# Kernel optimization log

Measured on AMD Instinct MI355X. Metric: run time of the kernel, lower is better.

## Reference

```python
import jax, jax.numpy as jnp
import numpy as np

DN = ('NHWC', 'HWIO', 'NHWC')
EPS = 1e-3  # Keras BatchNormalization default epsilon


def conv2d(x, w):
    return jax.lax.conv_general_dilated(x, w, (1, 1), 'SAME', dimension_numbers=DN)


def hard_sigmoid(x):
    # Keras ConvLSTM2D default recurrent_activation
    return jnp.clip(0.2 * x + 0.5, 0.0, 1.0)


def convlstm2d(x, Wx, Wh, b):
    """Keras ConvLSTM2D, return_sequences=True. x: (B,T,H,W,C).
    Wx: (3,3,C,4F) input kernel, Wh: (3,3,F,4F) recurrent kernel, b: (4F,).
    Gate order (Keras): i, f, c, o."""
    B, T, H, W, C = x.shape
    F = Wh.shape[2]
    # input-to-gate convs for all timesteps in one batched conv
    xg = conv2d(x.reshape(B * T, H, W, C), Wx) + b          # (B*T,H,W,4F)
    xg = xg.reshape(B, T, H, W, 4 * F).transpose(1, 0, 2, 3, 4)  # (T,B,H,W,4F)

    def step(carry, xg_t):
        h, c = carry
        g = xg_t + conv2d(h, Wh)                            # (B,H,W,4F)
        i, f, cc, o = jnp.split(g, 4, axis=-1)
        i = hard_sigmoid(i)
        f = hard_sigmoid(f)
        o = hard_sigmoid(o)
        c = f * c + i * jnp.tanh(cc)
        h = o * jnp.tanh(c)
        return (h, c), h

    h0 = jnp.zeros((B, H, W, F), x.dtype)
    (_, _), hs = jax.lax.scan(step, (h0, h0), xg)           # hs: (T,B,H,W,F)
    return hs.transpose(1, 0, 2, 3, 4)


def batchnorm(x, gamma, beta):
    # training-mode BN over all axes except channel (last)
    mu = x.mean(axis=(0, 1, 2, 3), keepdims=True)
    var = x.var(axis=(0, 1, 2, 3), keepdims=True)
    return gamma * (x - mu) * jax.lax.rsqrt(var + EPS) + beta


def setup_inputs() -> dict:
    key = jax.random.key(0)
    B, T, H, W, C = 4, 8, 16, 16, 256
    F = 256
    ks = jax.random.split(key, 10)
    s = 0.02
    inp = {
        'input_tensor': jax.random.normal(ks[0], (B, T, H, W, C), jnp.float32),
        'Wx1': jax.random.normal(ks[1], (3, 3, C, 4 * F), jnp.float32) * s,
        'Wh1': jax.random.normal(ks[2], (3, 3, F, 4 * F), jnp.float32) * s,
        'b1': jnp.zeros((4 * F,), jnp.float32),
        'g1': jnp.ones((F,), jnp.float32),
        'be1': jnp.zeros((F,), jnp.float32),
        'Wx2': jax.random.normal(ks[3], (3, 3, F, 4 * F), jnp.float32) * s,
        'Wh2': jax.random.normal(ks[4], (3, 3, F, 4 * F), jnp.float32) * s,
        'b2': jnp.zeros((4 * F,), jnp.float32),
        'g2': jnp.ones((F,), jnp.float32),
        'be2': jnp.zeros((F,), jnp.float32),
        'Wx3': jax.random.normal(ks[5], (3, 3, F, 4 * F), jnp.float32) * s,
        'Wh3': jax.random.normal(ks[6], (3, 3, F, 4 * F), jnp.float32) * s,
        'b3': jnp.zeros((4 * F,), jnp.float32),
        'g3': jnp.ones((F,), jnp.float32),
        'be3': jnp.zeros((F,), jnp.float32),
    }
    return inp


def reference(input_tensor, Wx1, Wh1, b1, g1, be1,
              Wx2, Wh2, b2, g2, be2,
              Wx3, Wh3, b3, g3, be3):
    x = batchnorm(convlstm2d(input_tensor, Wx1, Wh1, b1), g1, be1)
    x = batchnorm(convlstm2d(x, Wx2, Wh2, b2), g2, be2)
    x = batchnorm(convlstm2d(x, Wx3, Wh3, b3), g3, be3)
    return x
```

## Files before the change

### kernel.cpp

```cpp
#include <hip/hip_runtime.h>

#define HW      256
#define COUT    1024
#define TSTEPS  8
#define BN_EPS  1e-3f
#define KTOT    2304

typedef unsigned short u16;
typedef unsigned int   u32;
typedef __attribute__((ext_vector_type(8))) _Float16 v8h;
typedef __attribute__((ext_vector_type(4))) float v4f;

__device__ __forceinline__ u16 f2h(float x) {
    _Float16 h = (_Float16)x; return *(u16*)&h;
}
__device__ __forceinline__ float h2f(u16 u) {
    _Float16 h = *(_Float16*)&u; return (float)h;
}
__device__ __forceinline__ float hsig(float x) {
    return fminf(fmaxf(0.2f * x + 0.5f, 0.f), 1.f);
}

typedef __attribute__((address_space(1))) const unsigned int gas_u32;
typedef __attribute__((address_space(3))) unsigned int las_u32;
__device__ __forceinline__ void gl16(const void* g, void* l) {
    __builtin_amdgcn_global_load_lds((gas_u32*)g, (las_u32*)l, 16, 0, 0);
}

__global__ __launch_bounds__(256, 2) void conv_big_k(
    const u16* __restrict__ apad,
    const u16* __restrict__ wT,
    const float* __restrict__ bias,
    u16* __restrict__ out)
{
    constexpr int KQ = 36;
    __shared__ u16 lds[2 * 16384];

    const int bid = blockIdx.x;
    const int xcd = bid & 7, idx = bid >> 3;
    const int by = (xcd >> 1) * 2 + (idx & 1);
    const int bx = (xcd & 1) * 32 + (idx >> 1);
    const int m0 = bx * 128, n0 = by * 128;
    const int tid = threadIdx.x, lane = tid & 63, w = tid >> 6;
    const int wr = w >> 1, wc = w & 1;
    const int lr = lane >> 3;
    const int g  = (lane & 7) ^ lr;
    const int fr = lane & 15, kc = lane >> 4;

    const char* a_src[4];
    #pragma unroll
    for (int i = 0; i < 4; ++i) {
        int m = m0 + w * 32 + i * 8 + lr;
        int img = m >> 8, pix = m & 255, yy = pix >> 4, xx = pix & 15;
        a_src[i] = (const char*)apad + ((((long)img * 18 + yy) * 18 + xx) * 256 + g * 8) * 2;
    }
    const char* b_src[4];
    #pragma unroll
    for (int i = 0; i < 4; ++i) {
        int n = n0 + w * 32 + i * 8 + lr;
        b_src[i] = (const char*)wT + ((long)n * KTOT + g * 8) * 2;
    }

    int aro[4][2], bro[4][2];
    #pragma unroll
    for (int mi = 0; mi < 4; ++mi) {
        int rl = wr * 64 + mi * 16 + fr;
        #pragma unroll
        for (int ks = 0; ks < 2; ++ks)
            aro[mi][ks] = rl * 128 + ((((ks << 2) | kc) ^ (fr & 7)) << 4);
    }
    #pragma unroll
    for (int ni = 0; ni < 4; ++ni) {
        int nr = wc * 64 + ni * 16 + fr;
        #pragma unroll
        for (int ks = 0; ks < 2; ++ks)
            bro[ni][ks] = 16384 + nr * 128 + ((((ks << 2) | kc) ^ (fr & 7)) << 4);
    }

    v4f acc[4][4];
    #pragma unroll
    for (int mi = 0; mi < 4; ++mi)
        #pragma unroll
        for (int ni = 0; ni < 4; ++ni) acc[mi][ni] = (v4f)0.f;

#define STAGE_B(J) { int j_ = (J); int dxy = j_ >> 2, c64 = j_ & 3;           \
    int dy = (dxy * 11) >> 5; int dx = dxy - dy * 3;                          \
    int aoff = ((dy * 18 + dx) * 256 + c64 * 64) * 2; int boff = j_ * 128;    \
    char* base = (char*)lds + (j_ & 1) * 32768;                               \
    _Pragma("unroll") for (int i = 0; i < 4; ++i)                             \
        gl16(a_src[i] + aoff, base + (w * 32 + i * 8) * 128);                 \
    _Pragma("unroll") for (int i = 0; i < 4; ++i)                             \
        gl16(b_src[i] + boff, base + 16384 + (w * 32 + i * 8) * 128); }

#define COMPUTE_B(J) { const char* base = (const char*)lds + ((J) & 1) * 32768; \
    v8h af[4][2], bf[4][2];                                                   \
    _Pragma("unroll") for (int mi = 0; mi < 4; ++mi)                          \
        _Pragma("unroll") for (int ks = 0; ks < 2; ++ks)                      \
            af[mi][ks] = *(const v8h*)(base + aro[mi][ks]);                   \
    _Pragma("unroll") for (int ni = 0; ni < 4; ++ni)                          \
        _Pragma("unroll") for (int ks = 0; ks < 2; ++ks)                      \
            bf[ni][ks] = *(const v8h*)(base + bro[ni][ks]);                   \
    __builtin_amdgcn_s_setprio(1);                                            \
    _Pragma("unroll") for (int ks = 0; ks < 2; ++ks)                          \
    _Pragma("unroll") for (int mi = 0; mi < 4; ++mi)                          \
    _Pragma("unroll") for (int ni = 0; ni < 4; ++ni)                          \
        acc[mi][ni] = __builtin_amdgcn_mfma_f32_16x16x32_f16(af[mi][ks], bf[ni][ks], acc[mi][ni], 0, 0, 0); \
    __builtin_amdgcn_s_setprio(0); }

    STAGE_B(0);
    for (int kq = 0; kq < KQ - 1; ++kq) {
        asm volatile("s_waitcnt vmcnt(0)" ::: "memory");
        __builtin_amdgcn_s_barrier();
        __builtin_amdgcn_sched_barrier(0);
        STAGE_B(kq + 1);
        COMPUTE_B(kq);
    }
    asm volatile("s_waitcnt vmcnt(0)" ::: "memory");
    __builtin_amdgcn_s_barrier();
    __builtin_amdgcn_sched_barrier(0);
    COMPUTE_B(KQ - 1);
#undef STAGE_B
#undef COMPUTE_B

    #pragma unroll
    for (int mi = 0; mi < 4; ++mi) {
        #pragma unroll
        for (int ni = 0; ni < 4; ++ni) {
            int mrow = m0 + wr * 64 + mi * 16 + ((lane >> 4) << 2);
            int ncol = n0 + wc * 64 + ni * 16 + fr;
            float b0 = bias[(ncol & 3) * 256 + (ncol >> 2)];
            #pragma unroll
            for (int r = 0; r < 4; ++r)
                out[(long)(mrow + r) * COUT + ncol] = f2h(acc[mi][ni][r] + b0);
        }
    }
}

__global__ __launch_bounds__(256) void rec_fused_k(
    const u16* __restrict__ ph_in,
    const u16* __restrict__ wTf,
    const u16* __restrict__ xg,
    float* __restrict__ cbuf,
    float* __restrict__ hs,
    u16* __restrict__ ph_out,
    int t)
{
    __shared__ u16 lds[3 * 4096];

    const int bid = blockIdx.x;
    const int by = (bid & 7) * 2 + ((bid >> 3) & 1);
    const int bx = bid >> 4;
    const int m0 = bx * 64, n0 = by * 64;
    const int tid = threadIdx.x, lane = tid & 63, w = tid >> 6;
    const int lr = lane >> 3, g = (lane & 7) ^ lr;
    const int fr = lane & 15, kc = lane >> 4;

    const char* a_src[2];
    #pragma unroll
    for (int i = 0; i < 2; ++i) {
        int m = m0 + w * 16 + i * 8 + lr;
        int img = m >> 8, pix = m & 255, yy = pix >> 4, xx = pix & 15;
        a_src[i] = (const char*)ph_in + ((((long)img * 18 + yy) * 18 + xx) * 256 + g * 8) * 2;
    }
    const char* b_base = (const char*)wTf + ((long)(by * 4 + w) * 72) * 1024 + lane * 16;

    int aro[4][2];
    #pragma unroll
    for (int mi = 0; mi < 4; ++mi)
        #pragma unroll
        for (int ks = 0; ks < 2; ++ks)
            aro[mi][ks] = (mi * 16 + fr) * 128 + ((((ks << 2) | kc) ^ (fr & 7)) << 4);

    v4f acc0 = (v4f)0.f, acc1 = (v4f)0.f, acc2 = (v4f)0.f, acc3 = (v4f)0.f;
    v8h b0x, b0y, b1x, b1y;

#define STAGE_A(J) { int j_ = (J); int dxy = j_ >> 2, c64 = j_ & 3;           \
    int dy = (dxy * 11) >> 5; int dx = dxy - dy * 3;                          \
    int aoff = ((dy * 18 + dx) * 256 + c64 * 64) * 2;                         \
    char* dst = (char*)lds + (j_ % 3) * 8192 + (w * 16) * 128;                \
    gl16(a_src[0] + aoff, dst); gl16(a_src[1] + aoff, dst + 1024); }

#define LDB(J, RX, RY) { RX = *(const v8h*)(b_base + (2 * (J)) * 1024);       \
                         RY = *(const v8h*)(b_base + (2 * (J) + 1) * 1024); }

#define COMPUTE(J, RX, RY) { const char* base = (const char*)lds + ((J) % 3) * 8192; \
    v8h af0 = *(const v8h*)(base + aro[0][0]);                                \
    v8h af1 = *(const v8h*)(base + aro[1][0]);                                \
    v8h af2 = *(const v8h*)(base + aro[2][0]);                                \
    v8h af3 = *(const v8h*)(base + aro[3][0]);                                \
    v8h ag0 = *(const v8h*)(base + aro[0][1]);                                \
    v8h ag1 = *(const v8h*)(base + aro[1][1]);                                \
    v8h ag2 = *(const v8h*)(base + aro[2][1]);                                \
    v8h ag3 = *(const v8h*)(base + aro[3][1]);                                \
    __builtin_amdgcn_s_setprio(1);                                            \
    acc0 = __builtin_amdgcn_mfma_f32_16x16x32_f16(af0, RX, acc0, 0, 0, 0);    \
    acc1 = __builtin_amdgcn_mfma_f32_16x16x32_f16(af1, RX, acc1, 0, 0, 0);    \
    acc2 = __builtin_amdgcn_mfma_f32_16x16x32_f16(af2, RX, acc2, 0, 0, 0);    \
    acc3 = __builtin_amdgcn_mfma_f32_16x16x32_f16(af3, RX, acc3, 0, 0, 0);    \
    acc0 = __builtin_amdgcn_mfma_f32_16x16x32_f16(ag0, RY, acc0, 0, 0, 0);    \
    acc1 = __builtin_amdgcn_mfma_f32_16x16x32_f16(ag1, RY, acc1, 0, 0, 0);    \
    acc2 = __builtin_amdgcn_mfma_f32_16x16x32_f16(ag2, RY, acc2, 0, 0, 0);    \
    acc3 = __builtin_amdgcn_mfma_f32_16x16x32_f16(ag3, RY, acc3, 0, 0, 0);    \
    __builtin_amdgcn_s_setprio(0); }

    STAGE_A(0); LDB(0, b0x, b0y); STAGE_A(1);
    for (int j = 0; j < 17; ++j) {
        int kq = 2 * j;
        asm volatile("s_waitcnt vmcnt(2)" ::: "memory");
        __builtin_amdgcn_s_barrier();
        __builtin_amdgcn_sched_barrier(0);
        LDB(kq + 1, b1x, b1y); STAGE_A(kq + 2);
        COMPUTE(kq, b0x, b0y);
        asm volatile("s_waitcnt vmcnt(2)" ::: "memory");
        __builtin_amdgcn_s_barrier();
        __builtin_amdgcn_sched_barrier(0);
        LDB(kq + 2, b0x, b0y); STAGE_A(kq + 3);
        COMPUTE(kq + 1, b1x, b1y);
    }
    asm volatile("s_waitcnt vmcnt(2)" ::: "memory");
    __builtin_amdgcn_s_barrier();
    __builtin_amdgcn_sched_barrier(0);
    LDB(35, b1x, b1y);
    COMPUTE(34, b0x, b0y);
    asm volatile("s_waitcnt vmcnt(0)" ::: "memory");
    __builtin_amdgcn_s_barrier();
    __builtin_amdgcn_sched_barrier(0);
    COMPUTE(35, b1x, b1y);
#undef STAGE_A
#undef LDB
#undef COMPUTE

    v4f accA[4] = {acc0, acc1, acc2, acc3};
    const bool gl0 = lane & 1, gl1 = lane & 2;
    #pragma unroll
    for (int mi = 0; mi < 4; ++mi) {
        float V0 = accA[mi][0], V1 = accA[mi][1];
        float V2 = accA[mi][2], V3 = accA[mi][3];
        float x0 = __shfl_xor(V0, 1), x1 = __shfl_xor(V1, 1);
        float x2 = __shfl_xor(V2, 1), x3 = __shfl_xor(V3, 1);
        float a0 = gl0 ? x1 : V0;
        float a1 = gl0 ? V1 : x0;
        float a2 = gl0 ? x3 : V2;
        float a3 = gl0 ? V3 : x2;
        float s0 = __shfl_xor(a0, 2), s1 = __shfl_xor(a1, 2);
        float s2 = __shfl_xor(a2, 2), s3 = __shfl_xor(a3, 2);
        float Ti = gl1 ? s2 : a0;
        float Tf = gl1 ? s3 : a1;
        float Tc = gl1 ? a2 : s0;
        float To = gl1 ? a3 : s1;

        int row = m0 + mi * 16 + ((lane >> 4) << 2) + (lane & 3);
        int f4  = n0 + w * 16 + (lane & 12);
        int img = row >> 8, pix = row & 255, fch = f4 >> 2;
        long xrow = ((long)(img * TSTEPS + t) * HW + pix);
        uint2 xb = *(const uint2*)&xg[xrow * COUT + f4];
        float pi = Ti + h2f((u16)(xb.x & 0xffff));
        float pf = Tf + h2f((u16)(xb.x >> 16));
        float pc = Tc + h2f((u16)(xb.y & 0xffff));
        float po = To + h2f((u16)(xb.y >> 16));
        long cidx = (long)row * 256 + fch;
        float c = hsig(pf) * cbuf[cidx] + hsig(pi) * tanhf(pc);
        float h = hsig(po) * tanhf(c);
        cbuf[cidx] = c;
        hs[xrow * 256 + fch] = h;
        int yy = pix >> 4, xx = pix & 15;
        ph_out[(((long)img * 18 + yy + 1) * 18 + xx + 1) * 256 + fch] = f2h(h);
    }
}

__global__ __launch_bounds__(256) void gates0_k(
    const u16* __restrict__ xg, float* __restrict__ cbuf,
    float* __restrict__ hs, u16* __restrict__ ph_out)
{
    int idx = blockIdx.x * 256 + threadIdx.x;
    int fch = idx & 255, row = idx >> 8;
    int img = row >> 8, pix = row & 255;
    long xrow = (long)(img * TSTEPS) * HW + pix;
    uint2 xb = *(const uint2*)&xg[xrow * COUT + fch * 4];
    float pi = h2f((u16)(xb.x & 0xffff));
    float pc = h2f((u16)(xb.y & 0xffff));
    float po = h2f((u16)(xb.y >> 16));
    float c = hsig(pi) * tanhf(pc);
    float h = hsig(po) * tanhf(c);
    cbuf[(long)row * 256 + fch] = c;
    hs[xrow * 256 + fch] = h;
    int yy = pix >> 4, xx = pix & 15;
    ph_out[(((long)img * 18 + yy + 1) * 18 + xx + 1) * 256 + fch] = f2h(h);
}

__global__ __launch_bounds__(256) void wprep_k(const float* __restrict__ w,
                                               u16* __restrict__ wT)
{
    int k0 = blockIdx.x * 32;
    int np = blockIdx.y * 256 + threadIdx.x;
    int n  = (np & 3) * 256 + (np >> 2);
    u32 pk[16];
    #pragma unroll
    for (int kk = 0; kk < 32; kk += 2) {
        float a = w[(long)(k0 + kk) * COUT + n];
        float b = w[(long)(k0 + kk + 1) * COUT + n];
        pk[kk >> 1] = (u32)f2h(a) | ((u32)f2h(b) << 16);
    }
    uint4* dst = (uint4*)&wT[(long)np * KTOT + k0];
    dst[0] = make_uint4(pk[0], pk[1], pk[2], pk[3]);
    dst[1] = make_uint4(pk[4], pk[5], pk[6], pk[7]);
    dst[2] = make_uint4(pk[8], pk[9], pk[10], pk[11]);
    dst[3] = make_uint4(pk[12], pk[13], pk[14], pk[15]);
}

__global__ __launch_bounds__(256) void wprep_frag_k(const float* __restrict__ w,
                                                    u16* __restrict__ wTf)
{
    int kq = blockIdx.x;
    int nf = blockIdx.y * 4 + (threadIdx.x >> 6);
    int l  = threadIdx.x & 63;
    int np = nf * 16 + (l & 15);
    int n  = (np & 3) * 256 + (np >> 2);
    int k0 = kq * 32 + (l >> 4) * 8;
    u32 pk[4];
    #pragma unroll
    for (int e = 0; e < 8; e += 2) {
        float a = w[(long)(k0 + e) * COUT + n];
        float b = w[(long)(k0 + e + 1) * COUT + n];
        pk[e >> 1] = (u32)f2h(a) | ((u32)f2h(b) << 16);
    }
    *(uint4*)&wTf[((long)(nf * 72) + kq) * 512 + l * 8] =
        make_uint4(pk[0], pk[1], pk[2], pk[3]);
}

__global__ __launch_bounds__(256) void convert_x_k(const float* __restrict__ x,
                                                   u16* __restrict__ padx)
{
    int q = blockIdx.x * 256 + threadIdx.x;
    int e0 = q * 4;
    int f = e0 & 255, pix = (e0 >> 8) & 255, img = e0 >> 16;
    float4 v = ((const float4*)x)[q];
    int yy = pix >> 4, xx = pix & 15;
    long o = (((long)img * 18 + yy + 1) * 18 + xx + 1) * 256 + f;
    u32 lo = (u32)f2h(v.x) | ((u32)f2h(v.y) << 16);
    u32 hi = (u32)f2h(v.z) | ((u32)f2h(v.w) << 16);
    *(uint2*)&padx[o] = make_uint2(lo, hi);
}

__global__ __launch_bounds__(256) void bn_stats1_k(
    const float* __restrict__ x, float* __restrict__ partial)
{
    const int tid = threadIdx.x;
    const int blk = blockIdx.x;
    float s = 0.f, s2 = 0.f;
    const long base = (long)blk * 128 * 256;
    #pragma unroll 8
    for (int gi = 0; gi < 128; ++gi) {
        float v = x[base + gi * 256 + tid];
        s += v; s2 += v * v;
    }
    partial[blk * 512 + tid]       = s;
    partial[blk * 512 + 256 + tid] = s2;
}

__global__ __launch_bounds__(256) void bn_stats2_k(
    const float* __restrict__ partial, const float* __restrict__ gamma,
    const float* __restrict__ beta, float* __restrict__ stats)
{
    const int f = threadIdx.x;
    float s = 0.f, s2 = 0.f;
    #pragma unroll 8
    for (int b = 0; b < 64; ++b) {
        s  += partial[b * 512 + f];
        s2 += partial[b * 512 + 256 + f];
    }
    const float inv_n = 1.f / 8192.f;
    float mu  = s * inv_n;
    float var = s2 * inv_n - mu * mu;
    float sc  = gamma[f] * rsqrtf(var + BN_EPS);
    stats[f]       = sc;
    stats[256 + f] = beta[f] - mu * sc;
}

__global__ __launch_bounds__(256) void bn_apply_k(
    const float* __restrict__ x, const float* __restrict__ stats,
    u16* __restrict__ padx, float* __restrict__ out)
{
    const int q = blockIdx.x * 256 + threadIdx.x;
    const int e0 = q * 4;
    const int f = e0 & 255, pix = (e0 >> 8) & 255, img = e0 >> 16;
    float4 v  = ((const float4*)x)[q];
    float4 sc = *(const float4*)(stats + f);
    float4 sh = *(const float4*)(stats + 256 + f);
    v.x = v.x * sc.x + sh.x;
    v.y = v.y * sc.y + sh.y;
    v.z = v.z * sc.z + sh.z;
    v.w = v.w * sc.w + sh.w;
    if (out) ((float4*)out)[q] = v;
    if (padx) {
        int yy = pix >> 4, xx = pix & 15;
        long o = (((long)img * 18 + yy + 1) * 18 + xx + 1) * 256 + f;
        u32 lo = (u32)f2h(v.x) | ((u32)f2h(v.y) << 16);
        u32 hi = (u32)f2h(v.z) | ((u32)f2h(v.w) << 16);
        *(uint2*)&padx[o] = make_uint2(lo, hi);
    }
}

extern "C" void kernel_launch(void* const* d_in, const int* in_sizes, int n_in,
                              void* d_out, int out_size, void* d_ws, size_t ws_size,
                              hipStream_t stream)
{
    const float* x0    = (const float*)d_in[0];
    const float* Wx[3] = {(const float*)d_in[1], (const float*)d_in[6],  (const float*)d_in[11]};
    const float* Wh[3] = {(const float*)d_in[2], (const float*)d_in[7],  (const float*)d_in[12]};
    const float* bb[3] = {(const float*)d_in[3], (const float*)d_in[8],  (const float*)d_in[13]};
    const float* gg[3] = {(const float*)d_in[4], (const float*)d_in[9],  (const float*)d_in[14]};
    const float* be[3] = {(const float*)d_in[5], (const float*)d_in[10], (const float*)d_in[15]};

    float* ws    = (float*)d_ws;
    u16*  xg     = (u16*)ws;
    float* cbuf  = ws   + 4194304;
    float* hs    = cbuf + 262144;
    float* part  = hs   + 2097152;
    float* stats = part + 262144;
    u16*  pad_x  = (u16*)(stats + 512);
    u16*  pad_h  = pad_x + 2654208;
    u16*  wTx    = pad_h + 663552;
    u16*  wTf    = wTx   + 2359296;
    const long PHN = 331776;

    hipMemsetAsync(pad_x, 0, 2654208 * sizeof(u16), stream);
    hipMemsetAsync(pad_h, 0, 2 * PHN * sizeof(u16), stream);
    hipLaunchKernelGGL(convert_x_k, dim3(2048), dim3(256), 0, stream, x0, pad_x);

    for (int l = 0; l < 3; ++l) {
        hipLaunchKernelGGL(wprep_k, dim3(72, 4), dim3(256), 0, stream, Wx[l], wTx);
        hipLaunchKernelGGL(wprep_frag_k, dim3(72, 16), dim3(256), 0, stream, Wh[l], wTf);

        hipLaunchKernelGGL(conv_big_k, dim3(512), dim3(256), 0, stream,
            pad_x, wTx, bb[l], xg);

        hipLaunchKernelGGL(gates0_k, dim3(1024), dim3(256), 0, stream,
            xg, cbuf, hs, pad_h + PHN);

        for (int t = 1; t < TSTEPS; ++t) {
            hipLaunchKernelGGL(rec_fused_k, dim3(256), dim3(256), 0, stream,
                pad_h + (t & 1) * PHN, wTf, xg, cbuf, hs,
                pad_h + ((t & 1) ^ 1) * PHN, t);
        }

        hipLaunchKernelGGL(bn_stats1_k, dim3(64), dim3(256), 0, stream, hs, part);
        hipLaunchKernelGGL(bn_stats2_k, dim3(1), dim3(256), 0, stream, part, gg[l], be[l], stats);
        hipLaunchKernelGGL(bn_apply_k, dim3(2048), dim3(256), 0, stream, hs, stats,
            (l < 2) ? pad_x : (u16*)nullptr, (l == 2) ? (float*)d_out : (float*)nullptr);
    }
}
```

Measured before the change: 554.2 us.

## Halve recurrent tile M to double grid, deepen B-prefetch pipeline in conv

The recurrent fused kernel's tile shrinks from 64x64 to 32x64 rows, so the grid grows from 256 to 512 blocks and fills more compute units. The 4 waves are rearranged as 2x2, each computing 16 rows by 32 columns. Weight fragments are now triple-buffered in registers with a prefetch distance of two K-steps, and launch bounds ask for 2 blocks per CU. The big input conv's main loop now issues the next stage's loads before waiting, with a partial vmcnt(8) wait and an extra barrier, so loads overlap the current compute. In exchange, each block re-reads the weights for half as many rows, and there are more barriers per K-step.

Result: faster. 541.8 us (-2.2%).

```diff
diff --git a/kernel.cpp b/kernel.cpp
--- a/kernel.cpp
+++ b/kernel.cpp
@@ -108,17 +108,15 @@
     __builtin_amdgcn_s_setprio(0); }
 
     STAGE_B(0);
-    for (int kq = 0; kq < KQ - 1; ++kq) {
-        asm volatile("s_waitcnt vmcnt(0)" ::: "memory");
+    for (int kq = 0; kq < KQ; ++kq) {
+        int jj = kq + 1 < KQ ? kq + 1 : KQ - 1;
+        __builtin_amdgcn_s_barrier();
+        STAGE_B(jj);
+        asm volatile("s_waitcnt vmcnt(8)" ::: "memory");
         __builtin_amdgcn_s_barrier();
         __builtin_amdgcn_sched_barrier(0);
-        STAGE_B(kq + 1);
         COMPUTE_B(kq);
     }
-    asm volatile("s_waitcnt vmcnt(0)" ::: "memory");
-    __builtin_amdgcn_s_barrier();
-    __builtin_amdgcn_sched_barrier(0);
-    COMPUTE_B(KQ - 1);
 #undef STAGE_B
 #undef COMPUTE_B
 
@@ -136,7 +134,7 @@
     }
 }
 
-__global__ __launch_bounds__(256) void rec_fused_k(
+__global__ __launch_bounds__(256, 2) void rec_fused_k(
     const u16* __restrict__ ph_in,
     const u16* __restrict__ wTf,
     const u16* __restrict__ xg,
@@ -145,97 +143,81 @@
     u16* __restrict__ ph_out,
     int t)
 {
-    __shared__ u16 lds[3 * 4096];
+    __shared__ u16 lds[3 * 2048];
 
     const int bid = blockIdx.x;
     const int by = (bid & 7) * 2 + ((bid >> 3) & 1);
     const int bx = bid >> 4;
-    const int m0 = bx * 64, n0 = by * 64;
+    const int m0 = bx * 32, n0 = by * 64;
     const int tid = threadIdx.x, lane = tid & 63, w = tid >> 6;
-    const int lr = lane >> 3, g = (lane & 7) ^ lr;
+    const int wr = w >> 1, wc = w & 1;
     const int fr = lane & 15, kc = lane >> 4;
 
-    const char* a_src[2];
-    #pragma unroll
-    for (int i = 0; i < 2; ++i) {
-        int m = m0 + w * 16 + i * 8 + lr;
+    const char* a_src;
+    {
+        int rt = tid >> 3;
+        int gg = (lane & 7) ^ (rt & 7);
+        int m = m0 + rt;
         int img = m >> 8, pix = m & 255, yy = pix >> 4, xx = pix & 15;
-        a_src[i] = (const char*)ph_in + ((((long)img * 18 + yy) * 18 + xx) * 256 + g * 8) * 2;
-    }
-    const char* b_base = (const char*)wTf + ((long)(by * 4 + w) * 72) * 1024 + lane * 16;
-
-    int aro[4][2];
-    #pragma unroll
-    for (int mi = 0; mi < 4; ++mi)
-        #pragma unroll
-        for (int ks = 0; ks < 2; ++ks)
-            aro[mi][ks] = (mi * 16 + fr) * 128 + ((((ks << 2) | kc) ^ (fr & 7)) << 4);
-
-    v4f acc0 = (v4f)0.f, acc1 = (v4f)0.f, acc2 = (v4f)0.f, acc3 = (v4f)0.f;
-    v8h b0x, b0y, b1x, b1y;
+        a_src = (const char*)ph_in + ((((long)img * 18 + yy) * 18 + xx) * 256 + gg * 8) * 2;
+    }
+    const char* b_base0 = (const char*)wTf + ((long)(by * 4 + wc * 2 + 0) * 72) * 1024 + lane * 16;
+    const char* b_base1 = (const char*)wTf + ((long)(by * 4 + wc * 2 + 1) * 72) * 1024 + lane * 16;
+
+    int aro[2];
+    #pragma unroll
+    for (int ks = 0; ks < 2; ++ks)
+        aro[ks] = (wr * 16 + fr) * 128 + ((((ks << 2) | kc) ^ (fr & 7)) << 4);
+
+    v4f acc0 = (v4f)0.f, acc1 = (v4f)0.f;
 
 #define STAGE_A(J) { int j_ = (J); int dxy = j_ >> 2, c64 = j_ & 3;           \
     int dy = (dxy * 11) >> 5; int dx = dxy - dy * 3;                          \
     int aoff = ((dy * 18 + dx) * 256 + c64 * 64) * 2;                         \
-    char* dst = (char*)lds + (j_ % 3) * 8192 + (w * 16) * 128;                \
-    gl16(a_src[0] + aoff, dst); gl16(a_src[1] + aoff, dst + 1024); }
-
-#define LDB(J, RX, RY) { RX = *(const v8h*)(b_base + (2 * (J)) * 1024);       \
-                         RY = *(const v8h*)(b_base + (2 * (J) + 1) * 1024); }
-
-#define COMPUTE(J, RX, RY) { const char* base = (const char*)lds + ((J) % 3) * 8192; \
-    v8h af0 = *(const v8h*)(base + aro[0][0]);                                \
-    v8h af1 = *(const v8h*)(base + aro[1][0]);                                \
-    v8h af2 = *(const v8h*)(base + aro[2][0]);                                \
-    v8h af3 = *(const v8h*)(base + aro[3][0]);                                \
-    v8h ag0 = *(const v8h*)(base + aro[0][1]);                                \
-    v8h ag1 = *(const v8h*)(base + aro[1][1]);                                \
-    v8h ag2 = *(const v8h*)(base + aro[2][1]);                                \
-    v8h ag3 = *(const v8h*)(base + aro[3][1]);                                \
+    gl16(a_src + aoff, (char*)lds + (j_ % 3) * 4096 + w * 1024); }
+
+#define LDB(J, R00, R01, R10, R11) {                                          \
+    R00 = *(const v8h*)(b_base0 + (2 * (J)) * 1024);                          \
+    R01 = *(const v8h*)(b_base0 + (2 * (J) + 1) * 1024);                      \
+    R10 = *(const v8h*)(b_base1 + (2 * (J)) * 1024);                          \
+    R11 = *(const v8h*)(b_base1 + (2 * (J) + 1) * 1024); }
+
+#define BODY(KQ, C00, C01, C10, C11, L00, L01, L10, L11) {                    \
+    int kq_ = (KQ); int jj_ = kq_ + 2 < 36 ? kq_ + 2 : 35;                    \
+    asm volatile("s_waitcnt vmcnt(5)" ::: "memory");                          \
+    __builtin_amdgcn_s_barrier();                                             \
+    __builtin_amdgcn_sched_barrier(0);                                        \
+    LDB(jj_, L00, L01, L10, L11);                                             \
+    STAGE_A(jj_);                                                             \
+    const char* base_ = (const char*)lds + (kq_ % 3) * 4096;                  \
+    v8h af0_ = *(const v8h*)(base_ + aro[0]);                                 \
+    v8h af1_ = *(const v8h*)(base_ + aro[1]);                                 \
     __builtin_amdgcn_s_setprio(1);                                            \
-    acc0 = __builtin_amdgcn_mfma_f32_16x16x32_f16(af0, RX, acc0, 0, 0, 0);    \
-    acc1 = __builtin_amdgcn_mfma_f32_16x16x32_f16(af1, RX, acc1, 0, 0, 0);    \
-    acc2 = __builtin_amdgcn_mfma_f32_16x16x32_f16(af2, RX, acc2, 0, 0, 0);    \
-    acc3 = __builtin_amdgcn_mfma_f32_16x16x32_f16(af3, RX, acc3, 0, 0, 0);    \
-    acc0 = __builtin_amdgcn_mfma_f32_16x16x32_f16(ag0, RY, acc0, 0, 0, 0);    \
-    acc1 = __builtin_amdgcn_mfma_f32_16x16x32_f16(ag1, RY, acc1, 0, 0, 0);    \
-    acc2 = __builtin_amdgcn_mfma_f32_16x16x32_f16(ag2, RY, acc2, 0, 0, 0);    \
-    acc3 = __builtin_amdgcn_mfma_f32_16x16x32_f16(ag3, RY, acc3, 0, 0, 0);    \
+    acc0 = __builtin_amdgcn_mfma_f32_16x16x32_f16(af0_, C00, acc0, 0, 0, 0);  \
+    acc1 = __builtin_amdgcn_mfma_f32_16x16x32_f16(af0_, C10, acc1, 0, 0, 0);  \
+    acc0 = __builtin_amdgcn_mfma_f32_16x16x32_f16(af1_, C01, acc0, 0, 0, 0);  \
+    acc1 = __builtin_amdgcn_mfma_f32_16x16x32_f16(af1_, C11, acc1, 0, 0, 0);  \
     __builtin_amdgcn_s_setprio(0); }
 
-    STAGE_A(0); LDB(0, b0x, b0y); STAGE_A(1);
-    for (int j = 0; j < 17; ++j) {
-        int kq = 2 * j;
-        asm volatile("s_waitcnt vmcnt(2)" ::: "memory");
-        __builtin_amdgcn_s_barrier();
-        __builtin_amdgcn_sched_barrier(0);
-        LDB(kq + 1, b1x, b1y); STAGE_A(kq + 2);
-        COMPUTE(kq, b0x, b0y);
-        asm volatile("s_waitcnt vmcnt(2)" ::: "memory");
-        __builtin_amdgcn_s_barrier();
-        __builtin_amdgcn_sched_barrier(0);
-        LDB(kq + 2, b0x, b0y); STAGE_A(kq + 3);
-        COMPUTE(kq + 1, b1x, b1y);
-    }
-    asm volatile("s_waitcnt vmcnt(2)" ::: "memory");
-    __builtin_amdgcn_s_barrier();
-    __builtin_amdgcn_sched_barrier(0);
-    LDB(35, b1x, b1y);
-    COMPUTE(34, b0x, b0y);
-    asm volatile("s_waitcnt vmcnt(0)" ::: "memory");
-    __builtin_amdgcn_s_barrier();
-    __builtin_amdgcn_sched_barrier(0);
-    COMPUTE(35, b1x, b1y);
+    v8h A00, A01, A10, A11, B00, B01, B10, B11, C00, C01, C10, C11;
+    LDB(0, A00, A01, A10, A11); STAGE_A(0);
+    LDB(1, B00, B01, B10, B11); STAGE_A(1);
+    for (int j = 0; j < 12; ++j) {
+        int k0 = 3 * j;
+        BODY(k0,     A00, A01, A10, A11, C00, C01, C10, C11);
+        BODY(k0 + 1, B00, B01, B10, B11, A00, A01, A10, A11);
+        BODY(k0 + 2, C00, C01, C10, C11, B00, B01, B10, B11);
+    }
 #undef STAGE_A
 #undef LDB
-#undef COMPUTE
-
-    v4f accA[4] = {acc0, acc1, acc2, acc3};
+#undef BODY
+
+    v4f accA[2] = {acc0, acc1};
     const bool gl0 = lane & 1, gl1 = lane & 2;
     #pragma unroll
-    for (int mi = 0; mi < 4; ++mi) {
-        float V0 = accA[mi][0], V1 = accA[mi][1];
-        float V2 = accA[mi][2], V3 = accA[mi][3];
+    for (int ni = 0; ni < 2; ++ni) {
+        float V0 = accA[ni][0], V1 = accA[ni][1];
+        float V2 = accA[ni][2], V3 = accA[ni][3];
         float x0 = __shfl_xor(V0, 1), x1 = __shfl_xor(V1, 1);
         float x2 = __shfl_xor(V2, 1), x3 = __shfl_xor(V3, 1);
         float a0 = gl0 ? x1 : V0;
@@ -249,8 +231,8 @@
         float Tc = gl1 ? a2 : s0;
         float To = gl1 ? a3 : s1;
 
-        int row = m0 + mi * 16 + ((lane >> 4) << 2) + (lane & 3);
-        int f4  = n0 + w * 16 + (lane & 12);
+        int row = m0 + wr * 16 + ((lane >> 4) << 2) + (lane & 3);
+        int f4  = n0 + wc * 32 + ni * 16 + (lane & 12);
         int img = row >> 8, pix = row & 255, fch = f4 >> 2;
         long xrow = ((long)(img * TSTEPS + t) * HW + pix);
         uint2 xb = *(const uint2*)&xg[xrow * COUT + f4];
@@ -439,7 +421,7 @@
             xg, cbuf, hs, pad_h + PHN);
 
         for (int t = 1; t < TSTEPS; ++t) {
-            hipLaunchKernelGGL(rec_fused_k, dim3(256), dim3(256), 0, stream,
+            hipLaunchKernelGGL(rec_fused_k, dim3(512), dim3(256), 0, stream,
                 pad_h + (t & 1) * PHN, wTf, xg, cbuf, hs,
                 pad_h + ((t & 1) ^ 1) * PHN, t);
         }
```
